# Kernel optimization log

Hardware: AMD Instinct MI355X
Metric: run time of the kernel (lower is better)

## Reference

```python
import jax, jax.numpy as jnp
import numpy as np

ATTN = 128

def _gelu(x):
    return jax.nn.gelu(x, approximate=False)

def _mlp3(x, W1, b1, W2, b2, W3, b3):
    h = _gelu(x @ W1.T + b1)
    h = _gelu(h @ W2.T + b2)
    return h @ W3.T + b3

def setup_inputs() -> dict:
    key = jax.random.key(0)
    ks = jax.random.split(key, 32)
    B, K, M, C = 128, 64, 2048, 32
    QD, AD, H = 128, 128, 256
    s = 0.02
    d = {}
    d['g'] = jax.random.normal(ks[0], (B, K, 3), dtype=jnp.float32)
    d['query'] = jax.random.normal(ks[1], (M, QD), dtype=jnp.float32) * s
    d['qW'] = jax.random.normal(ks[2], (AD, QD), dtype=jnp.float32) * s
    d['qb'] = jnp.zeros((AD,), jnp.float32)
    d['kW'] = jax.random.normal(ks[3], (AD, 1), dtype=jnp.float32) * s
    d['kb'] = jnp.zeros((AD,), jnp.float32)
    # global_mlp: K -> H -> H -> H
    d['gm_W1'] = jax.random.normal(ks[4], (H, K), dtype=jnp.float32) * s
    d['gm_b1'] = jnp.zeros((H,), jnp.float32)
    d['gm_W2'] = jax.random.normal(ks[5], (H, H), dtype=jnp.float32) * s
    d['gm_b2'] = jnp.zeros((H,), jnp.float32)
    d['gm_W3'] = jax.random.normal(ks[6], (H, H), dtype=jnp.float32) * s
    d['gm_b3'] = jnp.zeros((H,), jnp.float32)
    # point_mlp: (H+QD+1) -> H -> H -> H
    d['pm_W1'] = jax.random.normal(ks[7], (H, H + QD + 1), dtype=jnp.float32) * s
    d['pm_b1'] = jnp.zeros((H,), jnp.float32)
    d['pm_W2'] = jax.random.normal(ks[8], (H, H), dtype=jnp.float32) * s
    d['pm_b2'] = jnp.zeros((H,), jnp.float32)
    d['pm_W3'] = jax.random.normal(ks[9], (H, H), dtype=jnp.float32) * s
    d['pm_b3'] = jnp.zeros((H,), jnp.float32)
    d['tW'] = jax.random.normal(ks[10], (C, H), dtype=jnp.float32) * s
    d['tb'] = jnp.zeros((C,), jnp.float32)
    d['wW'] = jax.random.normal(ks[11], (1, H), dtype=jnp.float32) * s
    d['wb'] = jnp.zeros((1,), jnp.float32)
    d['cW'] = jax.random.normal(ks[12], (1, H), dtype=jnp.float32) * s
    d['cb'] = jnp.zeros((1,), jnp.float32)
    return d

def reference(g, query, qW, qb, kW, kb,
              gm_W1, gm_b1, gm_W2, gm_b2, gm_W3, gm_b3,
              pm_W1, pm_b1, pm_W2, pm_b2, pm_W3, pm_b3,
              tW, tb, wW, wb, cW, cb):
    B, K, _ = g.shape
    M = query.shape[0]
    inv = jnp.linalg.norm(g, axis=-1)                    # (B,K)
    Q = query @ qW.T + qb                                # (M,AD)
    Kk = inv[..., None] * kW[:, 0] + kb                  # (B,K,AD) Linear(1->AD)
    scores = jnp.einsum('md,bkd->bmk', Q, Kk) / jnp.sqrt(jnp.float32(Q.shape[-1]))
    A = jax.nn.softmax(scores, axis=-1)                  # (B,M,K)
    y = jnp.einsum('bmk,bkd->bmd', A, g)                 # (B,M,3)
    global_s = _mlp3(inv, gm_W1, gm_b1, gm_W2, gm_b2, gm_W3, gm_b3)  # (B,H)
    attended_inv = jnp.einsum('bmk,bk->bm', A, inv)      # (B,M)
    s_in = jnp.concatenate([
        jnp.broadcast_to(global_s[:, None, :], (B, M, global_s.shape[-1])),
        jnp.broadcast_to(query[None], (B, M, query.shape[-1])),
        attended_inv[..., None],
    ], axis=-1)                                          # (B,M,H+QD+1)
    s = _mlp3(s_in, pm_W1, pm_b1, pm_W2, pm_b2, pm_W3, pm_b3)  # (B,M,H)
    type_logits = s @ tW.T + tb                          # (B,M,C)
    weight_logits = (s @ wW.T + wb)[..., 0]              # (B,M)
    gate = jnp.clip(jax.nn.sigmoid(s @ cW.T + cb), 0.0, 1.0)  # (B,M,1)
    y = y * gate
    return (y, type_logits, weight_logits)
```

## Files before the change

### kernel.cpp

```cpp
#include <hip/hip_runtime.h>
#include <hip/hip_bf16.h>
#include <math.h>


typedef __attribute__((ext_vector_type(8))) short short8;
typedef __attribute__((ext_vector_type(4))) float f32x4;

__device__ __forceinline__ unsigned short bf16_rne(float f){
    union { float f; unsigned u; } v; v.f = f;
    return (unsigned short)((v.u + 0x7FFFu + ((v.u >> 16) & 1u)) >> 16);
}
__device__ __forceinline__ unsigned pk_bf16(float a, float b){
    float2 t; t.x = a; t.y = b;
    __hip_bfloat162 h = __float22bfloat162_rn(t);
    union { __hip_bfloat162 h; unsigned u; } cv; cv.h = h;
    return cv.u;
}

__device__ __forceinline__ float gelu_f(float x){
    float z  = x * 0.70710678118654752f;
    float az = fabsf(z);
    float t  = __builtin_amdgcn_rcpf(1.0f + 0.3275911f * az);
    float p  = t*(0.254829592f + t*(-0.284496736f + t*(1.421413741f + t*(-1.453152027f + t*1.061405429f))));
    float e  = __expf(-az*az);
    float er = copysignf(1.0f - p*e, z);
    return 0.5f * x * (1.0f + er);
}

__device__ __forceinline__ float gelu_fast(float x){
    float x2 = x*x;
    float p  = fmaf(x2, -0.1029433f, -2.3022082f);
    float u  = x*p;
    float e  = __builtin_amdgcn_exp2f(u);
    float r  = __builtin_amdgcn_rcpf(1.0f + e);
    return x*r;
}

__global__ void k_pre1(const float* __restrict__ g, const float* __restrict__ qW,
                       const float* __restrict__ qb, const float* __restrict__ kW,
                       const float* __restrict__ query, const float* __restrict__ pmW1,
                       const float* __restrict__ pmW2, const float* __restrict__ pmW3,
                       const float* __restrict__ pmb3,
                       const float* __restrict__ gmW1, const float* __restrict__ gmW2,
                       const float* __restrict__ gmW3,
                       const float* __restrict__ tW, const float* __restrict__ tb,
                       const float* __restrict__ wW, const float* __restrict__ wb,
                       const float* __restrict__ cW, const float* __restrict__ cb,
                       float* __restrict__ invg, float* __restrict__ vg, float* __restrict__ s0g,
                       unsigned short* __restrict__ w2b, unsigned short* __restrict__ wheadb,
                       float* __restrict__ bheadg,
                       unsigned short* __restrict__ w1qb, unsigned short* __restrict__ queryb,
                       float* __restrict__ gmW1t, float* __restrict__ gmW2t,
                       float* __restrict__ gmW3t, float* __restrict__ w1gt,
                       float* __restrict__ w385g) {
    const int bid = blockIdx.x, tid = threadIdx.x;
    if (bid < 32) {
        int idx = bid*256 + tid;
        const float* p = g + idx*3;
        invg[idx] = sqrtf(p[0]*p[0] + p[1]*p[1] + p[2]*p[2]);
    } else if (bid == 32) {
        if (tid < 128) {
            float acc = 0.f;
            for (int d = 0; d < 128; ++d) acc += qW[d*128 + tid] * kW[d];
            vg[tid] = acc;
            if (tid == 0) {
                float s = 0.f;
                for (int d = 0; d < 128; ++d) s += qb[d] * kW[d];
                *s0g = s;
            }
        }
    } else if (bid < 97) {
        int o = (bid - 33)*1024 + tid*4;
        float4 x = *(const float4*)&pmW2[o];
        union { unsigned short u[4]; uint2 v; } r;
        r.u[0] = bf16_rne(x.x); r.u[1] = bf16_rne(x.y);
        r.u[2] = bf16_rne(x.z); r.u[3] = bf16_rne(x.w);
        *(uint2*)&w2b[o] = r.v;
    } else if (bid < 131) {
        __shared__ float hw[256];
        int c = bid - 97;
        const float* src = (c < 32) ? (tW + c*256) : ((c == 32) ? wW : cW);
        hw[tid] = src[tid];
        __syncthreads();
        float acc = 0.f;
        for (int j = 0; j < 256; ++j) acc += hw[j] * pmW3[j*256 + tid];
        wheadb[c*256 + tid] = bf16_rne(acc);
        if (tid == 0) {
            float bacc = (c < 32) ? tb[c] : ((c == 32) ? wb[0] : cb[0]);
            for (int j = 0; j < 256; ++j) bacc += hw[j] * pmb3[j];
            bheadg[c] = bacc;
        }
    } else if (bid < 163) {
        int o = (bid - 131)*1024 + tid*4;
        int n = o >> 7, k = o & 127;
        union { unsigned short u[4]; uint2 v; } r;
        #pragma unroll
        for (int i = 0; i < 4; ++i) r.u[i] = bf16_rne(pmW1[n*385 + 256 + k + i]);
        *(uint2*)&w1qb[o] = r.v;
    } else if (bid < 227) {
        int base = (bid - 163)*4096 + tid*4;
        #pragma unroll
        for (int it = 0; it < 4; ++it) {
            int o = base + it*1024;
            float4 x = *(const float4*)&query[o];
            union { unsigned short u[4]; uint2 v; } r;
            r.u[0] = bf16_rne(x.x); r.u[1] = bf16_rne(x.y);
            r.u[2] = bf16_rne(x.z); r.u[3] = bf16_rne(x.w);
            *(uint2*)&queryb[o] = r.v;
        }
    } else if (bid < 291) {
        int o = (bid - 227)*1024 + tid*4;
        int i = o >> 8, j = o & 255;
        float4 r = { gmW2[j*256+i], gmW2[(j+1)*256+i], gmW2[(j+2)*256+i], gmW2[(j+3)*256+i] };
        *(float4*)&gmW2t[o] = r;
    } else if (bid < 355) {
        int o = (bid - 291)*1024 + tid*4;
        int i = o >> 8, j = o & 255;
        float4 r = { gmW3[j*256+i], gmW3[(j+1)*256+i], gmW3[(j+2)*256+i], gmW3[(j+3)*256+i] };
        *(float4*)&gmW3t[o] = r;
    } else if (bid < 419) {
        int o = (bid - 355)*1024 + tid*4;
        int i = o >> 8, j = o & 255;
        float4 r = { pmW1[j*385+i], pmW1[(j+1)*385+i], pmW1[(j+2)*385+i], pmW1[(j+3)*385+i] };
        *(float4*)&w1gt[o] = r;
    } else if (bid < 435) {
        int o = (bid - 419)*1024 + tid*4;
        int k = o >> 8, j = o & 255;
        float4 r = { gmW1[j*64+k], gmW1[(j+1)*64+k], gmW1[(j+2)*64+k], gmW1[(j+3)*64+k] };
        *(float4*)&gmW1t[o] = r;
    } else {
        w385g[tid] = pmW1[tid*385 + 384];
    }
}

__global__ void k_pre2(const float* __restrict__ query, const float* __restrict__ vg,
                       const float* __restrict__ s0g, const float* __restrict__ invg,
                       const float* __restrict__ gmW1t, const float* __restrict__ gmb1,
                       const float* __restrict__ gmW2t, const float* __restrict__ gmb2,
                       const float* __restrict__ gmW3t, const float* __restrict__ gmb3,
                       const float* __restrict__ w1gt, const float* __restrict__ pmb1,
                       const unsigned short* __restrict__ queryb,
                       const unsigned short* __restrict__ w1qb,
                       float* __restrict__ ag, float* __restrict__ u1g,
                       float* __restrict__ u2g) {
    const int bid = blockIdx.x, tid = threadIdx.x;
    if (bid < 8) {
        __shared__ float vs[128];
        if (tid < 128) vs[tid] = vg[tid];
        __syncthreads();
        int m = bid*256 + tid;
        const float4* qp = (const float4*)(query + m*128);
        float acc = *s0g;
        #pragma unroll 8
        for (int e4 = 0; e4 < 32; ++e4) {
            float4 q = qp[e4];
            acc += q.x*vs[e4*4] + q.y*vs[e4*4+1] + q.z*vs[e4*4+2] + q.w*vs[e4*4+3];
        }
        ag[m] = acc * 0.08838834764831845f;
    } else if (bid < 136) {
        __shared__ float s_in[64];
        __shared__ float s_h[256];
        __shared__ float s_h2[256];
        int b = bid - 8;
        if (tid < 64) s_in[tid] = invg[b*64 + tid];
        __syncthreads();
        float acc = gmb1[tid];
        #pragma unroll 8
        for (int k = 0; k < 64; ++k) acc += gmW1t[k*256 + tid] * s_in[k];
        s_h[tid] = gelu_f(acc);
        __syncthreads();
        acc = gmb2[tid];
        #pragma unroll 8
        for (int i = 0; i < 256; ++i) acc += gmW2t[i*256 + tid] * s_h[i];
        s_h2[tid] = gelu_f(acc);
        __syncthreads();
        acc = gmb3[tid];
        #pragma unroll 8
        for (int i = 0; i < 256; ++i) acc += gmW3t[i*256 + tid] * s_h2[i];
        __syncthreads();
        s_h[tid] = acc;
        __syncthreads();
        float u = pmb1[tid];
        #pragma unroll 8
        for (int i = 0; i < 256; ++i) u += w1gt[i*256 + tid] * s_h[i];
        u1g[b*256 + tid] = u;
    } else {
        const int m0 = (bid - 136)*64;
        const int w = tid >> 6, lane = tid & 63;
        const int q = lane >> 4, ln = lane & 15;
        f32x4 acc[4][4];
        #pragma unroll
        for (int mt = 0; mt < 4; ++mt)
            #pragma unroll
            for (int nt = 0; nt < 4; ++nt) acc[mt][nt] = (f32x4){0.f,0.f,0.f,0.f};
        #pragma unroll
        for (int kk = 0; kk < 4; ++kk) {
            const int kc = kk*32 + q*8;
            short8 afr[4], bfr[4];
            #pragma unroll
            for (int mt = 0; mt < 4; ++mt)
                afr[mt] = *(const short8*)&queryb[(m0 + mt*16 + ln)*128 + kc];
            #pragma unroll
            for (int nt = 0; nt < 4; ++nt)
                bfr[nt] = *(const short8*)&w1qb[(w*64 + nt*16 + ln)*128 + kc];
            #pragma unroll
            for (int mt = 0; mt < 4; ++mt)
                #pragma unroll
                for (int nt = 0; nt < 4; ++nt)
                    acc[mt][nt] = __builtin_amdgcn_mfma_f32_16x16x32_bf16(afr[mt], bfr[nt], acc[mt][nt], 0, 0, 0);
        }
        #pragma unroll
        for (int mt = 0; mt < 4; ++mt)
            #pragma unroll
            for (int nt = 0; nt < 4; ++nt) {
                const int n = w*64 + nt*16 + ln;
                #pragma unroll
                for (int rg = 0; rg < 4; ++rg)
                    u2g[(size_t)(m0 + mt*16 + q*4 + rg)*256 + n] = acc[mt][nt][rg];
            }
    }
}

__global__ __launch_bounds__(256, 4)
void k_main(const float* __restrict__ g,
            const float* __restrict__ invg, const float* __restrict__ ag,
            const float* __restrict__ u1g, const float* __restrict__ u2g,
            const float* __restrict__ w385g, const float* __restrict__ pmb2,
            const unsigned short* __restrict__ w2b, const unsigned short* __restrict__ wheadb,
            const float* __restrict__ bheadg, float* __restrict__ out) {
    __shared__ __align__(16) unsigned short hb[64*264];
    __shared__ __align__(16) float u1s[256], w385s[256], pmb2s[256];
    __shared__ float invs[64], gsl[192], ainv_s[64], y0s[192];

    const int tid = threadIdx.x;
    const int bid = blockIdx.x;
    const int b  = bid >> 5;
    const int m0 = (bid & 31) << 6;

    if (tid < 64)  invs[tid] = invg[b*64 + tid];
    if (tid < 192) gsl[tid]  = g[b*192 + tid];
    u1s[tid]   = u1g[b*256 + tid];
    w385s[tid] = w385g[tid];
    pmb2s[tid] = pmb2[tid];
    __syncthreads();

    {
        const int r = tid >> 2, sub = tid & 3;
        const float am = ag[m0 + r];
        const int kb = sub * 16;
        float mx = -1e30f;
        #pragma unroll
        for (int i = 0; i < 16; ++i) mx = fmaxf(mx, invs[kb + i] * am);
        #pragma unroll
        for (int d = 1; d < 4; d <<= 1) mx = fmaxf(mx, __shfl_xor(mx, d, 64));
        float den = 0.f, ai = 0.f, y0 = 0.f, y1 = 0.f, y2 = 0.f;
        #pragma unroll
        for (int i = 0; i < 16; ++i) {
            const int k = kb + i;
            const float iv = invs[k];
            const float e = __expf(iv * am - mx);
            den += e; ai += e * iv;
            y0 += e * gsl[k*3+0]; y1 += e * gsl[k*3+1]; y2 += e * gsl[k*3+2];
        }
        #pragma unroll
        for (int d = 1; d < 4; d <<= 1) {
            den += __shfl_xor(den, d, 64);
            ai  += __shfl_xor(ai , d, 64);
            y0  += __shfl_xor(y0 , d, 64);
            y1  += __shfl_xor(y1 , d, 64);
            y2  += __shfl_xor(y2 , d, 64);
        }
        if (sub == 0) {
            const float id = 1.0f / den;
            ainv_s[r] = ai * id;
            y0s[r*3+0] = y0*id; y0s[r*3+1] = y1*id; y0s[r*3+2] = y2*id;
        }
    }
    __syncthreads();

    {
        const int ln16 = tid & 15, rbase = tid >> 4;
        #pragma unroll
        for (int rr = 0; rr < 4; ++rr) {
            const int r = rr*16 + rbase;
            const float aiv = ainv_s[r];
            const float* u2p = u2g + (size_t)(m0 + r)*256;
            #pragma unroll
            for (int k = 0; k < 4; ++k) {
                const int c = ln16*4 + k*64;
                float4 x  = *(const float4*)&u2p[c];
                float4 uv = *(const float4*)&u1s[c];
                float4 wv = *(const float4*)&w385s[c];
                float g0 = gelu_fast(x.x + uv.x + aiv*wv.x);
                float g1 = gelu_fast(x.y + uv.y + aiv*wv.y);
                float g2 = gelu_fast(x.z + uv.z + aiv*wv.z);
                float g3 = gelu_fast(x.w + uv.w + aiv*wv.w);
                uint2 pk; pk.x = pk_bf16(g0, g1); pk.y = pk_bf16(g2, g3);
                *(uint2*)&hb[r*264 + c] = pk;
            }
        }
    }
    __syncthreads();

    const int w = tid >> 6, lane = tid & 63;
    const int q = lane >> 4, ln = lane & 15;

    f32x4 acc[4][4];
    #pragma unroll
    for (int mt = 0; mt < 4; ++mt)
        #pragma unroll
        for (int nt = 0; nt < 4; ++nt) acc[mt][nt] = (f32x4){0.f,0.f,0.f,0.f};

    {
        const unsigned short* w2p = w2b + (w*64 + ln)*256 + q*8;
        short8 bcur[4], bnxt[4];
        #pragma unroll
        for (int nt = 0; nt < 4; ++nt) bcur[nt] = *(const short8*)(w2p + nt*4096);
        #pragma unroll
        for (int kk = 0; kk < 8; ++kk) {
            if (kk < 7) {
                #pragma unroll
                for (int nt = 0; nt < 4; ++nt)
                    bnxt[nt] = *(const short8*)(w2p + nt*4096 + (kk+1)*32);
            }
            short8 afrag[4];
            const int kc = kk*32 + q*8;
            #pragma unroll
            for (int mt = 0; mt < 4; ++mt)
                afrag[mt] = *(const short8*)&hb[(mt*16 + ln)*264 + kc];
            #pragma unroll
            for (int mt = 0; mt < 4; ++mt)
                #pragma unroll
                for (int nt = 0; nt < 4; ++nt)
                    acc[mt][nt] = __builtin_amdgcn_mfma_f32_16x16x32_bf16(afrag[mt], bcur[nt], acc[mt][nt], 0, 0, 0);
            #pragma unroll
            for (int nt = 0; nt < 4; ++nt) bcur[nt] = bnxt[nt];
        }
    }
    __syncthreads();

    #pragma unroll
    for (int mt = 0; mt < 4; ++mt) {
        #pragma unroll
        for (int nt = 0; nt < 4; ++nt) {
            const int n = w*64 + nt*16 + ln;
            const float bb = pmb2s[n];
            const int r0 = mt*16 + q*4;
            float h0 = gelu_fast(acc[mt][nt][0] + bb);
            float h1 = gelu_fast(acc[mt][nt][1] + bb);
            float h2 = gelu_fast(acc[mt][nt][2] + bb);
            float h3 = gelu_fast(acc[mt][nt][3] + bb);
            unsigned p01 = pk_bf16(h0, h1);
            unsigned p23 = pk_bf16(h2, h3);
            hb[(r0+0)*264 + n] = (unsigned short)(p01 & 0xFFFF);
            hb[(r0+1)*264 + n] = (unsigned short)(p01 >> 16);
            hb[(r0+2)*264 + n] = (unsigned short)(p23 & 0xFFFF);
            hb[(r0+3)*264 + n] = (unsigned short)(p23 >> 16);
        }
    }

    const int cb2 = (ln < 2) ? (32 + ln) : 33;
    const unsigned short* whp = wheadb + q*8;
    short8 wf0 = *(const short8*)(whp +  ln      *256);
    short8 wf1 = *(const short8*)(whp + (16 + ln)*256);
    short8 wf2 = *(const short8*)(whp +  cb2     *256);
    __syncthreads();

    f32x4 accA0 = {0.f,0.f,0.f,0.f}, accA1 = {0.f,0.f,0.f,0.f}, accB = {0.f,0.f,0.f,0.f};
    const int rr = w*16 + ln;
    #pragma unroll
    for (int kk = 0; kk < 8; ++kk) {
        short8 wn0, wn1, wn2;
        if (kk < 7) {
            wn0 = *(const short8*)(whp +  ln      *256 + (kk+1)*32);
            wn1 = *(const short8*)(whp + (16 + ln)*256 + (kk+1)*32);
            wn2 = *(const short8*)(whp +  cb2     *256 + (kk+1)*32);
        }
        short8 bh = *(const short8*)&hb[rr*264 + kk*32 + q*8];
        accA0 = __builtin_amdgcn_mfma_f32_16x16x32_bf16(wf0, bh, accA0, 0, 0, 0);
        accA1 = __builtin_amdgcn_mfma_f32_16x16x32_bf16(wf1, bh, accA1, 0, 0, 0);
        accB  = __builtin_amdgcn_mfma_f32_16x16x32_bf16(wf2, bh, accB , 0, 0, 0);
        wf0 = wn0; wf1 = wn1; wf2 = wn2;
    }
    {
        const size_t row = (size_t)b*2048 + m0 + rr;
        const int c0 = q*4;
        f32x4 r0 = accA0 + *(const f32x4*)&bheadg[c0];
        f32x4 r1 = accA1 + *(const f32x4*)&bheadg[16 + c0];
        *(f32x4*)&out[786432 + row*32 + c0]      = r0;
        *(f32x4*)&out[786432 + row*32 + 16 + c0] = r1;
        if (q == 0) {
            out[9175040 + row] = accB[0] + bheadg[32];
            float gv = accB[1] + bheadg[33];
            float gt = 1.0f / (1.0f + __expf(-gv));
            gt = fminf(fmaxf(gt, 0.0f), 1.0f);
            float* yo = out + row*3;
            yo[0] = y0s[rr*3+0] * gt;
            yo[1] = y0s[rr*3+1] * gt;
            yo[2] = y0s[rr*3+2] * gt;
        }
    }
}

extern "C" void kernel_launch(void* const* d_in, const int* in_sizes, int n_in,
                              void* d_out, int out_size, void* d_ws, size_t ws_size,
                              hipStream_t stream) {
    const float* g     = (const float*)d_in[0];
    const float* query = (const float*)d_in[1];
    const float* qW    = (const float*)d_in[2];
    const float* qb    = (const float*)d_in[3];
    const float* kW    = (const float*)d_in[4];
    const float* gmW1  = (const float*)d_in[6];
    const float* gmb1  = (const float*)d_in[7];
    const float* gmW2  = (const float*)d_in[8];
    const float* gmb2  = (const float*)d_in[9];
    const float* gmW3  = (const float*)d_in[10];
    const float* gmb3  = (const float*)d_in[11];
    const float* pmW1  = (const float*)d_in[12];
    const float* pmb1  = (const float*)d_in[13];
    const float* pmW2  = (const float*)d_in[14];
    const float* pmb2  = (const float*)d_in[15];
    const float* pmW3  = (const float*)d_in[16];
    const float* pmb3  = (const float*)d_in[17];
    const float* tW    = (const float*)d_in[18];
    const float* tb    = (const float*)d_in[19];
    const float* wW    = (const float*)d_in[20];
    const float* wb    = (const float*)d_in[21];
    const float* cW    = (const float*)d_in[22];
    const float* cb    = (const float*)d_in[23];
    float* out = (float*)d_out;

    float* ws    = (float*)d_ws;
    float* invg  = ws;
    float* ag    = ws + 8192;
    float* vg    = ws + 10240;
    float* s0g   = ws + 10368;
    float* u1g   = ws + 10496;
    float* gmW1t = ws + 43264;
    float* gmW2t = ws + 59648;
    float* gmW3t = ws + 125184;
    float* w1gt  = ws + 190720;
    float* w385g = ws + 256256;
    float* bheadg= ws + 256512;
    unsigned short* w2b    = (unsigned short*)(ws + 256576);
    unsigned short* wheadb = (unsigned short*)(ws + 289344);
    unsigned short* w1qb   = (unsigned short*)(ws + 293696);
    unsigned short* queryb = (unsigned short*)(ws + 310080);
    float* u2g   = ws + 441152;

    hipLaunchKernelGGL(k_pre1, dim3(436), dim3(256), 0, stream,
                       g, qW, qb, kW, query, pmW1, pmW2, pmW3, pmb3,
                       gmW1, gmW2, gmW3,
                       tW, tb, wW, wb, cW, cb,
                       invg, vg, s0g, w2b, wheadb, bheadg,
                       w1qb, queryb, gmW1t, gmW2t, gmW3t, w1gt, w385g);
    hipLaunchKernelGGL(k_pre2, dim3(168), dim3(256), 0, stream,
                       query, vg, s0g, invg,
                       gmW1t, gmb1, gmW2t, gmb2, gmW3t, gmb3, w1gt, pmb1,
                       queryb, w1qb,
                       ag, u1g, u2g);
    hipLaunchKernelGGL(k_main, dim3(4096), dim3(256), 0, stream,
                       g, invg, ag, u1g, u2g, w385g, pmb2,
                       w2b, wheadb, bheadg, out);
}
```

Baseline: 269.6 us.

## Merge two preprocessing kernels into one and use MFMA for global MLP

Folds the two preprocessing launches into a single k_prep kernel. Each block recomputes the data it depends on (the v vector, norms, bf16 operands in shared memory), which removes the workspace round trips and transposed weight copies. The global MLP plus the first point-MLP projection now run as bf16 MFMA GEMMs over 64-batch tiles instead of scalar fp32 dot loops. This saves a launch and a dependency barrier, but it lowers the global branch to bf16 precision and has some blocks redo work redundantly, such as the qW·kW product in every ag block.

```diff
diff --git a/kernel.cpp b/kernel.cpp
--- a/kernel.cpp
+++ b/kernel.cpp
@@ -15,6 +15,22 @@
     __hip_bfloat162 h = __float22bfloat162_rn(t);
     union { __hip_bfloat162 h; unsigned u; } cv; cv.h = h;
     return cv.u;
+}
+__device__ __forceinline__ short8 cvt8_f4(const float* __restrict__ p){
+    float4 a = *(const float4*)p;
+    float4 b = *(const float4*)(p + 4);
+    short8 s;
+    s[0]=(short)bf16_rne(a.x); s[1]=(short)bf16_rne(a.y);
+    s[2]=(short)bf16_rne(a.z); s[3]=(short)bf16_rne(a.w);
+    s[4]=(short)bf16_rne(b.x); s[5]=(short)bf16_rne(b.y);
+    s[6]=(short)bf16_rne(b.z); s[7]=(short)bf16_rne(b.w);
+    return s;
+}
+__device__ __forceinline__ short8 cvt8_s(const float* __restrict__ p){
+    short8 s;
+    #pragma unroll
+    for (int i = 0; i < 8; ++i) s[i] = (short)bf16_rne(p[i]);
+    return s;
 }
 
 __device__ __forceinline__ float gelu_f(float x){
@@ -26,7 +42,6 @@
     float er = copysignf(1.0f - p*e, z);
     return 0.5f * x * (1.0f + er);
 }
-
 __device__ __forceinline__ float gelu_fast(float x){
     float x2 = x*x;
     float p  = fmaf(x2, -0.1029433f, -2.3022082f);
@@ -36,49 +51,41 @@
     return x*r;
 }
 
-__global__ void k_pre1(const float* __restrict__ g, const float* __restrict__ qW,
-                       const float* __restrict__ qb, const float* __restrict__ kW,
-                       const float* __restrict__ query, const float* __restrict__ pmW1,
-                       const float* __restrict__ pmW2, const float* __restrict__ pmW3,
-                       const float* __restrict__ pmb3,
-                       const float* __restrict__ gmW1, const float* __restrict__ gmW2,
-                       const float* __restrict__ gmW3,
-                       const float* __restrict__ tW, const float* __restrict__ tb,
-                       const float* __restrict__ wW, const float* __restrict__ wb,
-                       const float* __restrict__ cW, const float* __restrict__ cb,
-                       float* __restrict__ invg, float* __restrict__ vg, float* __restrict__ s0g,
-                       unsigned short* __restrict__ w2b, unsigned short* __restrict__ wheadb,
-                       float* __restrict__ bheadg,
-                       unsigned short* __restrict__ w1qb, unsigned short* __restrict__ queryb,
-                       float* __restrict__ gmW1t, float* __restrict__ gmW2t,
-                       float* __restrict__ gmW3t, float* __restrict__ w1gt,
-                       float* __restrict__ w385g) {
+__global__ __launch_bounds__(256)
+void k_prep(const float* __restrict__ g, const float* __restrict__ qW,
+            const float* __restrict__ qb, const float* __restrict__ kW,
+            const float* __restrict__ query, const float* __restrict__ pmW1,
+            const float* __restrict__ pmb1,
+            const float* __restrict__ pmW2, const float* __restrict__ pmW3,
+            const float* __restrict__ pmb3,
+            const float* __restrict__ gmW1, const float* __restrict__ gmb1,
+            const float* __restrict__ gmW2, const float* __restrict__ gmb2,
+            const float* __restrict__ gmW3, const float* __restrict__ gmb3,
+            const float* __restrict__ tW, const float* __restrict__ tb,
+            const float* __restrict__ wW, const float* __restrict__ wb,
+            const float* __restrict__ cW, const float* __restrict__ cb,
+            float* __restrict__ invg, float* __restrict__ ag,
+            float* __restrict__ u1g, float* __restrict__ u2g,
+            unsigned short* __restrict__ w2b, unsigned short* __restrict__ wheadb,
+            float* __restrict__ bheadg, float* __restrict__ w385g) {
+    __shared__ __align__(16) unsigned char smem[87040];
     const int bid = blockIdx.x, tid = threadIdx.x;
+    const int w = tid >> 6, lane = tid & 63, q = lane >> 4, ln = lane & 15;
+
     if (bid < 32) {
         int idx = bid*256 + tid;
         const float* p = g + idx*3;
         invg[idx] = sqrtf(p[0]*p[0] + p[1]*p[1] + p[2]*p[2]);
-    } else if (bid == 32) {
-        if (tid < 128) {
-            float acc = 0.f;
-            for (int d = 0; d < 128; ++d) acc += qW[d*128 + tid] * kW[d];
-            vg[tid] = acc;
-            if (tid == 0) {
-                float s = 0.f;
-                for (int d = 0; d < 128; ++d) s += qb[d] * kW[d];
-                *s0g = s;
-            }
-        }
-    } else if (bid < 97) {
-        int o = (bid - 33)*1024 + tid*4;
+    } else if (bid < 96) {
+        int o = (bid - 32)*1024 + tid*4;
         float4 x = *(const float4*)&pmW2[o];
         union { unsigned short u[4]; uint2 v; } r;
         r.u[0] = bf16_rne(x.x); r.u[1] = bf16_rne(x.y);
         r.u[2] = bf16_rne(x.z); r.u[3] = bf16_rne(x.w);
         *(uint2*)&w2b[o] = r.v;
-    } else if (bid < 131) {
-        __shared__ float hw[256];
-        int c = bid - 97;
+    } else if (bid < 130) {
+        float* hw = (float*)smem;
+        int c = bid - 96;
         const float* src = (c < 32) ? (tW + c*256) : ((c == 32) ? wW : cW);
         hw[tid] = src[tid];
         __syncthreads();
@@ -90,104 +97,173 @@
             for (int j = 0; j < 256; ++j) bacc += hw[j] * pmb3[j];
             bheadg[c] = bacc;
         }
-    } else if (bid < 163) {
-        int o = (bid - 131)*1024 + tid*4;
-        int n = o >> 7, k = o & 127;
-        union { unsigned short u[4]; uint2 v; } r;
-        #pragma unroll
-        for (int i = 0; i < 4; ++i) r.u[i] = bf16_rne(pmW1[n*385 + 256 + k + i]);
-        *(uint2*)&w1qb[o] = r.v;
-    } else if (bid < 227) {
-        int base = (bid - 163)*4096 + tid*4;
-        #pragma unroll
-        for (int it = 0; it < 4; ++it) {
-            int o = base + it*1024;
-            float4 x = *(const float4*)&query[o];
-            union { unsigned short u[4]; uint2 v; } r;
-            r.u[0] = bf16_rne(x.x); r.u[1] = bf16_rne(x.y);
-            r.u[2] = bf16_rne(x.z); r.u[3] = bf16_rne(x.w);
-            *(uint2*)&queryb[o] = r.v;
-        }
-    } else if (bid < 291) {
-        int o = (bid - 227)*1024 + tid*4;
-        int i = o >> 8, j = o & 255;
-        float4 r = { gmW2[j*256+i], gmW2[(j+1)*256+i], gmW2[(j+2)*256+i], gmW2[(j+3)*256+i] };
-        *(float4*)&gmW2t[o] = r;
-    } else if (bid < 355) {
-        int o = (bid - 291)*1024 + tid*4;
-        int i = o >> 8, j = o & 255;
-        float4 r = { gmW3[j*256+i], gmW3[(j+1)*256+i], gmW3[(j+2)*256+i], gmW3[(j+3)*256+i] };
-        *(float4*)&gmW3t[o] = r;
-    } else if (bid < 419) {
-        int o = (bid - 355)*1024 + tid*4;
-        int i = o >> 8, j = o & 255;
-        float4 r = { pmW1[j*385+i], pmW1[(j+1)*385+i], pmW1[(j+2)*385+i], pmW1[(j+3)*385+i] };
-        *(float4*)&w1gt[o] = r;
-    } else if (bid < 435) {
-        int o = (bid - 419)*1024 + tid*4;
-        int k = o >> 8, j = o & 255;
-        float4 r = { gmW1[j*64+k], gmW1[(j+1)*64+k], gmW1[(j+2)*64+k], gmW1[(j+3)*64+k] };
-        *(float4*)&gmW1t[o] = r;
-    } else {
+    } else if (bid == 130) {
         w385g[tid] = pmW1[tid*385 + 384];
-    }
-}
-
-__global__ void k_pre2(const float* __restrict__ query, const float* __restrict__ vg,
-                       const float* __restrict__ s0g, const float* __restrict__ invg,
-                       const float* __restrict__ gmW1t, const float* __restrict__ gmb1,
-                       const float* __restrict__ gmW2t, const float* __restrict__ gmb2,
-                       const float* __restrict__ gmW3t, const float* __restrict__ gmb3,
-                       const float* __restrict__ w1gt, const float* __restrict__ pmb1,
-                       const unsigned short* __restrict__ queryb,
-                       const unsigned short* __restrict__ w1qb,
-                       float* __restrict__ ag, float* __restrict__ u1g,
-                       float* __restrict__ u2g) {
-    const int bid = blockIdx.x, tid = threadIdx.x;
-    if (bid < 8) {
-        __shared__ float vs[128];
-        if (tid < 128) vs[tid] = vg[tid];
-        __syncthreads();
-        int m = bid*256 + tid;
+    } else if (bid < 139) {
+        float* kws = (float*)smem;
+        float* vs  = kws + 128;
+        float* red = vs  + 128;
+        if (tid < 128) kws[tid] = kW[tid];
+        __syncthreads();
+        if (tid < 128) {
+            float acc = 0.f;
+            for (int d = 0; d < 128; ++d) acc += qW[d*128 + tid] * kws[d];
+            vs[tid] = acc;
+            red[tid] = qb[tid] * kws[tid];
+        }
+        __syncthreads();
+        float s0 = 0.f;
+        #pragma unroll 8
+        for (int i = 0; i < 128; ++i) s0 += red[i];
+        int m = (bid - 131)*256 + tid;
         const float4* qp = (const float4*)(query + m*128);
-        float acc = *s0g;
+        float acc = s0;
         #pragma unroll 8
         for (int e4 = 0; e4 < 32; ++e4) {
-            float4 q = qp[e4];
-            acc += q.x*vs[e4*4] + q.y*vs[e4*4+1] + q.z*vs[e4*4+2] + q.w*vs[e4*4+3];
+            float4 qv = qp[e4];
+            acc += qv.x*vs[e4*4] + qv.y*vs[e4*4+1] + qv.z*vs[e4*4+2] + qv.w*vs[e4*4+3];
         }
         ag[m] = acc * 0.08838834764831845f;
-    } else if (bid < 136) {
-        __shared__ float s_in[64];
-        __shared__ float s_h[256];
-        __shared__ float s_h2[256];
-        int b = bid - 8;
-        if (tid < 64) s_in[tid] = invg[b*64 + tid];
-        __syncthreads();
-        float acc = gmb1[tid];
-        #pragma unroll 8
-        for (int k = 0; k < 64; ++k) acc += gmW1t[k*256 + tid] * s_in[k];
-        s_h[tid] = gelu_f(acc);
-        __syncthreads();
-        acc = gmb2[tid];
-        #pragma unroll 8
-        for (int i = 0; i < 256; ++i) acc += gmW2t[i*256 + tid] * s_h[i];
-        s_h2[tid] = gelu_f(acc);
-        __syncthreads();
-        acc = gmb3[tid];
-        #pragma unroll 8
-        for (int i = 0; i < 256; ++i) acc += gmW3t[i*256 + tid] * s_h2[i];
-        __syncthreads();
-        s_h[tid] = acc;
-        __syncthreads();
-        float u = pmb1[tid];
-        #pragma unroll 8
-        for (int i = 0; i < 256; ++i) u += w1gt[i*256 + tid] * s_h[i];
-        u1g[b*256 + tid] = u;
+    } else if (bid < 141) {
+        unsigned short* invA = (unsigned short*)smem;
+        unsigned short* hA   = (unsigned short*)(smem + 9216);
+        unsigned short* hB   = (unsigned short*)(smem + 43008);
+        const int b0 = (bid - 139)*64;
+        for (int i = tid; i < 4096; i += 256) {
+            int r = i >> 6, k = i & 63;
+            const float* p = g + ((size_t)(b0 + r)*64 + k)*3;
+            invA[r*72 + k] = bf16_rne(sqrtf(p[0]*p[0] + p[1]*p[1] + p[2]*p[2]));
+        }
+        __syncthreads();
+
+        f32x4 acc[4][4];
+        #pragma unroll
+        for (int mt = 0; mt < 4; ++mt)
+            #pragma unroll
+            for (int nt = 0; nt < 4; ++nt) acc[mt][nt] = (f32x4){0.f,0.f,0.f,0.f};
+        #pragma unroll
+        for (int kk = 0; kk < 2; ++kk) {
+            const int kc = kk*32 + q*8;
+            short8 af[4], bf_[4];
+            #pragma unroll
+            for (int mt = 0; mt < 4; ++mt) af[mt] = *(const short8*)&invA[(mt*16 + ln)*72 + kc];
+            #pragma unroll
+            for (int nt = 0; nt < 4; ++nt) bf_[nt] = cvt8_f4(gmW1 + (w*64 + nt*16 + ln)*64 + kc);
+            #pragma unroll
+            for (int mt = 0; mt < 4; ++mt)
+                #pragma unroll
+                for (int nt = 0; nt < 4; ++nt)
+                    acc[mt][nt] = __builtin_amdgcn_mfma_f32_16x16x32_bf16(af[mt], bf_[nt], acc[mt][nt], 0, 0, 0);
+        }
+        #pragma unroll
+        for (int mt = 0; mt < 4; ++mt)
+            #pragma unroll
+            for (int nt = 0; nt < 4; ++nt) {
+                const int n = w*64 + nt*16 + ln;
+                const float bb = gmb1[n];
+                #pragma unroll
+                for (int rg = 0; rg < 4; ++rg)
+                    hA[(mt*16 + q*4 + rg)*264 + n] = bf16_rne(gelu_f(acc[mt][nt][rg] + bb));
+            }
+        __syncthreads();
+        #pragma unroll
+        for (int mt = 0; mt < 4; ++mt)
+            #pragma unroll
+            for (int nt = 0; nt < 4; ++nt) acc[mt][nt] = (f32x4){0.f,0.f,0.f,0.f};
+        for (int kk = 0; kk < 8; ++kk) {
+            const int kc = kk*32 + q*8;
+            short8 af[4], bf_[4];
+            #pragma unroll
+            for (int mt = 0; mt < 4; ++mt) af[mt] = *(const short8*)&hA[(mt*16 + ln)*264 + kc];
+            #pragma unroll
+            for (int nt = 0; nt < 4; ++nt) bf_[nt] = cvt8_f4(gmW2 + (w*64 + nt*16 + ln)*256 + kc);
+            #pragma unroll
+            for (int mt = 0; mt < 4; ++mt)
+                #pragma unroll
+                for (int nt = 0; nt < 4; ++nt)
+                    acc[mt][nt] = __builtin_amdgcn_mfma_f32_16x16x32_bf16(af[mt], bf_[nt], acc[mt][nt], 0, 0, 0);
+        }
+        __syncthreads();
+        #pragma unroll
+        for (int mt = 0; mt < 4; ++mt)
+            #pragma unroll
+            for (int nt = 0; nt < 4; ++nt) {
+                const int n = w*64 + nt*16 + ln;
+                const float bb = gmb2[n];
+                #pragma unroll
+                for (int rg = 0; rg < 4; ++rg)
+                    hB[(mt*16 + q*4 + rg)*264 + n] = bf16_rne(gelu_f(acc[mt][nt][rg] + bb));
+            }
+        __syncthreads();
+        #pragma unroll
+        for (int mt = 0; mt < 4; ++mt)
+            #pragma unroll
+            for (int nt = 0; nt < 4; ++nt) acc[mt][nt] = (f32x4){0.f,0.f,0.f,0.f};
+        for (int kk = 0; kk < 8; ++kk) {
+            const int kc = kk*32 + q*8;
+            short8 af[4], bf_[4];
+            #pragma unroll
+            for (int mt = 0; mt < 4; ++mt) af[mt] = *(const short8*)&hB[(mt*16 + ln)*264 + kc];
+            #pragma unroll
+            for (int nt = 0; nt < 4; ++nt) bf_[nt] = cvt8_f4(gmW3 + (w*64 + nt*16 + ln)*256 + kc);
+            #pragma unroll
+            for (int mt = 0; mt < 4; ++mt)
+                #pragma unroll
+                for (int nt = 0; nt < 4; ++nt)
+                    acc[mt][nt] = __builtin_amdgcn_mfma_f32_16x16x32_bf16(af[mt], bf_[nt], acc[mt][nt], 0, 0, 0);
+        }
+        __syncthreads();
+        #pragma unroll
+        for (int mt = 0; mt < 4; ++mt)
+            #pragma unroll
+            for (int nt = 0; nt < 4; ++nt) {
+                const int n = w*64 + nt*16 + ln;
+                const float bb = gmb3[n];
+                #pragma unroll
+                for (int rg = 0; rg < 4; ++rg)
+                    hA[(mt*16 + q*4 + rg)*264 + n] = bf16_rne(acc[mt][nt][rg] + bb);
+            }
+        __syncthreads();
+        #pragma unroll
+        for (int mt = 0; mt < 4; ++mt)
+            #pragma unroll
+            for (int nt = 0; nt < 4; ++nt) acc[mt][nt] = (f32x4){0.f,0.f,0.f,0.f};
+        for (int kk = 0; kk < 8; ++kk) {
+            const int kc = kk*32 + q*8;
+            short8 af[4], bf_[4];
+            #pragma unroll
+            for (int mt = 0; mt < 4; ++mt) af[mt] = *(const short8*)&hA[(mt*16 + ln)*264 + kc];
+            #pragma unroll
+            for (int nt = 0; nt < 4; ++nt) bf_[nt] = cvt8_s(pmW1 + (size_t)(w*64 + nt*16 + ln)*385 + kc);
+            #pragma unroll
+            for (int mt = 0; mt < 4; ++mt)
+                #pragma unroll
+                for (int nt = 0; nt < 4; ++nt)
+                    acc[mt][nt] = __builtin_amdgcn_mfma_f32_16x16x32_bf16(af[mt], bf_[nt], acc[mt][nt], 0, 0, 0);
+        }
+        #pragma unroll
+        for (int mt = 0; mt < 4; ++mt)
+            #pragma unroll
+            for (int nt = 0; nt < 4; ++nt) {
+                const int n = w*64 + nt*16 + ln;
+                const float bb = pmb1[n];
+                #pragma unroll
+                for (int rg = 0; rg < 4; ++rg)
+                    u1g[(size_t)(b0 + mt*16 + q*4 + rg)*256 + n] = acc[mt][nt][rg] + bb;
+            }
     } else {
-        const int m0 = (bid - 136)*64;
-        const int w = tid >> 6, lane = tid & 63;
-        const int q = lane >> 4, ln = lane & 15;
+        unsigned short* qs = (unsigned short*)smem;
+        unsigned short* wsd = (unsigned short*)(smem + 17408);
+        const int m0 = (bid - 141)*64;
+        for (int i = tid; i < 64*128; i += 256) {
+            int r = i >> 7, c = i & 127;
+            qs[r*136 + c] = bf16_rne(query[(size_t)(m0 + r)*128 + c]);
+        }
+        for (int i = tid; i < 256*128; i += 256) {
+            int n = i >> 7, c = i & 127;
+            wsd[n*136 + c] = bf16_rne(pmW1[(size_t)n*385 + 256 + c]);
+        }
+        __syncthreads();
         f32x4 acc[4][4];
         #pragma unroll
         for (int mt = 0; mt < 4; ++mt)
@@ -196,18 +272,16 @@
         #pragma unroll
         for (int kk = 0; kk < 4; ++kk) {
             const int kc = kk*32 + q*8;
-            short8 afr[4], bfr[4];
-            #pragma unroll
-            for (int mt = 0; mt < 4; ++mt)
-                afr[mt] = *(const short8*)&queryb[(m0 + mt*16 + ln)*128 + kc];
-            #pragma unroll
-            for (int nt = 0; nt < 4; ++nt)
-                bfr[nt] = *(const short8*)&w1qb[(w*64 + nt*16 + ln)*128 + kc];
-            #pragma unroll
-            for (int mt = 0; mt < 4; ++mt)
-                #pragma unroll
-                for (int nt = 0; nt < 4; ++nt)
-                    acc[mt][nt] = __builtin_amdgcn_mfma_f32_16x16x32_bf16(afr[mt], bfr[nt], acc[mt][nt], 0, 0, 0);
+            short8 af[4], bf_[4];
+            #pragma unroll
+            for (int mt = 0; mt < 4; ++mt) af[mt] = *(const short8*)&qs[(mt*16 + ln)*136 + kc];
+            #pragma unroll
+            for (int nt = 0; nt < 4; ++nt) bf_[nt] = *(const short8*)&wsd[(w*64 + nt*16 + ln)*136 + kc];
+            #pragma unroll
+            for (int mt = 0; mt < 4; ++mt)
+                #pragma unroll
+                for (int nt = 0; nt < 4; ++nt)
+                    acc[mt][nt] = __builtin_amdgcn_mfma_f32_16x16x32_bf16(af[mt], bf_[nt], acc[mt][nt], 0, 0, 0);
         }
         #pragma unroll
         for (int mt = 0; mt < 4; ++mt)
@@ -433,32 +507,18 @@
     float* ws    = (float*)d_ws;
     float* invg  = ws;
     float* ag    = ws + 8192;
-    float* vg    = ws + 10240;
-    float* s0g   = ws + 10368;
-    float* u1g   = ws + 10496;
-    float* gmW1t = ws + 43264;
-    float* gmW2t = ws + 59648;
-    float* gmW3t = ws + 125184;
-    float* w1gt  = ws + 190720;
-    float* w385g = ws + 256256;
-    float* bheadg= ws + 256512;
-    unsigned short* w2b    = (unsigned short*)(ws + 256576);
-    unsigned short* wheadb = (unsigned short*)(ws + 289344);
-    unsigned short* w1qb   = (unsigned short*)(ws + 293696);
-    unsigned short* queryb = (unsigned short*)(ws + 310080);
-    float* u2g   = ws + 441152;
-
-    hipLaunchKernelGGL(k_pre1, dim3(436), dim3(256), 0, stream,
-                       g, qW, qb, kW, query, pmW1, pmW2, pmW3, pmb3,
-                       gmW1, gmW2, gmW3,
+    float* u1g   = ws + 10240;
+    float* w385g = ws + 43008;
+    float* bheadg= ws + 43264;
+    unsigned short* w2b    = (unsigned short*)(ws + 43328);
+    unsigned short* wheadb = (unsigned short*)(ws + 76096);
+    float* u2g   = ws + 80448;
+
+    hipLaunchKernelGGL(k_prep, dim3(173), dim3(256), 0, stream,
+                       g, qW, qb, kW, query, pmW1, pmb1, pmW2, pmW3, pmb3,
+                       gmW1, gmb1, gmW2, gmb2, gmW3, gmb3,
                        tW, tb, wW, wb, cW, cb,
-                       invg, vg, s0g, w2b, wheadb, bheadg,
-                       w1qb, queryb, gmW1t, gmW2t, gmW3t, w1gt, w385g);
-    hipLaunchKernelGGL(k_pre2, dim3(168), dim3(256), 0, stream,
-                       query, vg, s0g, invg,
-                       gmW1t, gmb1, gmW2t, gmb2, gmW3t, gmb3, w1gt, pmb1,
-                       queryb, w1qb,
-                       ag, u1g, u2g);
+                       invg, ag, u1g, u2g, w2b, wheadb, bheadg, w385g);
     hipLaunchKernelGGL(k_main, dim3(4096), dim3(256), 0, stream,
                        g, invg, ag, u1g, u2g, w385g, pmb2,
                        w2b, wheadb, bheadg, out);
```

Result: faster. 255.4 us (-5.3%).
